# Performance work log

Measured on AMD Instinct MI355X. Metric: run time of the kernel, lower is better.

## Reference

```python
import jax, jax.numpy as jnp
import numpy as np

N = 4096
IN_F = 128
OUT_F = 64      # per-head out_features
HEADS = 4
ALPHA = 0.2     # LeakyReLU negative slope
NEG_FILL = -9e15


def setup_inputs() -> dict:
    key = jax.random.key(0)
    k_h, k_adj, k_W, k_a = jax.random.split(key, 4)
    h = jax.random.normal(k_h, (N, IN_F), dtype=jnp.float32)
    adj = jax.random.randint(k_adj, (N, N), 0, 2, dtype=jnp.int32)
    W = jax.random.normal(k_W, (IN_F, OUT_F * HEADS), dtype=jnp.float32) * 0.1
    a = jax.random.normal(k_a, (2 * OUT_F, 1), dtype=jnp.float32) * 0.1
    bias = jnp.zeros((OUT_F * HEADS,), dtype=jnp.float32)
    return {"h": h, "adj": adj, "W": W, "a": a, "bias": bias}


def reference(h, adj, W, a, bias):
    n = h.shape[0]
    Wh = (h @ W).reshape(n, HEADS, OUT_F)            # (N, H, F)
    # e_ij = leakyrelu(a_left . Wh_i + a_right . Wh_j)  (decomposed outer sum;
    # same math as concat([Wh_i, Wh_j]) @ a in the original)
    a_left = a[:OUT_F, 0]                            # (F,)
    a_right = a[OUT_F:, 0]                           # (F,)
    left = jnp.einsum('nhf,f->nh', Wh, a_left)       # (N, H)
    right = jnp.einsum('nhf,f->nh', Wh, a_right)     # (N, H)
    mask = adj > 0                                   # (N, N)
    outs = []
    for head in range(HEADS):                        # small fixed loop over heads
        e = left[:, head, None] + right[None, :, head]          # (N, N)
        e = jnp.where(e >= 0, e, ALPHA * e)                      # LeakyReLU
        e = jnp.where(mask, e, NEG_FILL)
        attn = jax.nn.softmax(e, axis=1)                         # (N, N)
        outs.append(attn @ Wh[:, head, :])                       # (N, F)
    out = jnp.concatenate(outs, axis=1)              # concat=True -> (N, H*F)
    return out + bias
```

## Files before the change

kernel.cpp:

```cpp
#include <hip/hip_runtime.h>
#include <hip/hip_bf16.h>

#define NN 4096
#define IN_F 128
#define OUT_F 64
#define C_TOT 256
#define ALPHA 0.2f
#define LOG2E 1.4426950408889634f

typedef float f32x4 __attribute__((ext_vector_type(4)));
typedef float f32x2 __attribute__((ext_vector_type(2)));
typedef __bf16 bf16x8 __attribute__((ext_vector_type(8)));

__device__ __forceinline__ unsigned fmap(float f) {
    unsigned u = __float_as_uint(f);
    return (u >> 31) ? ~u : (u | 0x80000000u);
}
__device__ __forceinline__ float funmap(unsigned u) {
    return (u >> 31) ? __uint_as_float(u & 0x7FFFFFFFu) : __uint_as_float(~u);
}
__device__ __forceinline__ unsigned short bfbits(float x) {
    union { __bf16 b; unsigned short u; } t;
    t.b = (__bf16)x;
    return t.u;
}
__device__ __forceinline__ void gl16(const void* g, void* l) {
    __builtin_amdgcn_global_load_lds((const __attribute__((address_space(1))) void*)g,
                                     (__attribute__((address_space(3))) void*)l, 16, 0, 0);
}

__global__ __launch_bounds__(256) void k_mask(
    const int* __restrict__ adj, unsigned* __restrict__ mask,
    const float* __restrict__ W, const float* __restrict__ a,
    unsigned short* __restrict__ WTbf, float* __restrict__ uLR,
    unsigned int* __restrict__ Rmax)
{
    const int tid = threadIdx.x;
    const int lane = tid & 63, wv = tid >> 6;
    const int row = blockIdx.x * 4 + wv;
    const int* __restrict__ ar = adj + (size_t)row * NN;
    unsigned* __restrict__ mr = mask + (size_t)row * 128;
    for (int c = 0; c < 8; ++c) {
        const int j0 = c * 512;
        unsigned w = 0u;
#pragma unroll
        for (int k = 0; k < 8; ++k) {
            const unsigned long long bb = __ballot(ar[j0 + k * 64 + lane] > 0);
            const unsigned lo = (unsigned)bb, hi = (unsigned)(bb >> 32);
            if ((lane >> 1) == k) w = (lane & 1) ? hi : lo;
        }
        if (lane < 16) {
            const int wi = c * 16 + lane;
            mr[(wi & 3) * 32 + (wi >> 2)] = w;
        }
    }

    if (blockIdx.x < 32) {
        const int b = blockIdx.x;
        const int c = b * 8 + (tid & 7);
#pragma unroll
        for (int pass = 0; pass < 4; ++pass) {
            const int k = pass * 32 + (tid >> 3);
            WTbf[(size_t)c * IN_F + k] = bfbits(W[k * C_TOT + c]);
        }
        if (b == 0) {
            if (tid < 4) Rmax[tid] = 0u;
            for (int o = tid; o < 1024; o += 256) {
                const int k = o >> 3, j = o & 7;
                const int hd = j & 3, side = j >> 2;
                float s = 0.f;
                for (int f = 0; f < OUT_F; ++f)
                    s = fmaf(W[k * C_TOT + hd * OUT_F + f], a[side * OUT_F + f], s);
                uLR[k * 8 + side * 4 + hd] = s;
            }
        }
    }
}

__global__ __launch_bounds__(256) void k_prep(
    const float* __restrict__ hmat, const unsigned short* __restrict__ WTbf,
    const float* __restrict__ uLR, unsigned short* __restrict__ WhT,
    float* __restrict__ leftT, float* __restrict__ rightT,
    unsigned int* __restrict__ Rmax)
{
    __shared__ float hs[16][132];
    __shared__ float us[128][8];
    const int tid = threadIdx.x;
    const int rowbase = blockIdx.x * 16;

    ((float4*)us)[tid] = ((const float4*)uLR)[tid];
#pragma unroll
    for (int p = 0; p < 8; ++p) {
        const int idx = p * 256 + tid;
        hs[idx >> 7][idx & 127] = hmat[(size_t)rowbase * IN_F + idx];
    }
    __syncthreads();

    const int lane = tid & 63, wv = tid >> 6;
    const int m16 = lane & 15, kg = lane >> 4;

    if (wv == 0) {
        const int row = lane >> 2, hd = lane & 3;
        float aL = 0.f, aR = 0.f;
#pragma unroll
        for (int k = 0; k < 128; k += 4) {
            const float4 hv = *(const float4*)&hs[row][k];
            aL = fmaf(hv.x, us[k][hd],   fmaf(hv.y, us[k+1][hd],   fmaf(hv.z, us[k+2][hd],   fmaf(hv.w, us[k+3][hd],   aL))));
            aR = fmaf(hv.x, us[k][hd+4], fmaf(hv.y, us[k+1][hd+4], fmaf(hv.z, us[k+2][hd+4], fmaf(hv.w, us[k+3][hd+4], aR))));
        }
        leftT [hd * NN + rowbase + row] = aL;
        rightT[hd * NN + rowbase + row] = aR * LOG2E;
        float mx = aR;
#pragma unroll
        for (int s = 4; s < 64; s <<= 1) mx = fmaxf(mx, __shfl_xor(mx, s, 64));
        if (lane < 4) atomicMax(&Rmax[hd], fmap(mx));
    }

    bf16x8 afr[4];
#pragma unroll
    for (int ks = 0; ks < 4; ++ks) {
        const float4 lo = *(const float4*)&hs[m16][ks * 32 + kg * 8];
        const float4 hi = *(const float4*)&hs[m16][ks * 32 + kg * 8 + 4];
        bf16x8 v;
        v[0] = (__bf16)lo.x; v[1] = (__bf16)lo.y; v[2] = (__bf16)lo.z; v[3] = (__bf16)lo.w;
        v[4] = (__bf16)hi.x; v[5] = (__bf16)hi.y; v[6] = (__bf16)hi.z; v[7] = (__bf16)hi.w;
        afr[ks] = v;
    }

#pragma unroll
    for (int nt0 = 0; nt0 < 4; ++nt0) {
        const int col = (wv * 4 + nt0) * 16 + m16;
        f32x4 acc = (f32x4){0.f, 0.f, 0.f, 0.f};
#pragma unroll
        for (int ks = 0; ks < 4; ++ks) {
            union { uint4 u; bf16x8 v; } B;
            B.u = *(const uint4*)(WTbf + (size_t)col * IN_F + ks * 32 + kg * 8);
            acc = __builtin_amdgcn_mfma_f32_16x16x32_bf16(afr[ks], B.v, acc, 0, 0, 0);
        }
#pragma unroll
        for (int i = 0; i < 4; ++i)
            WhT[(size_t)col * NN + rowbase + kg * 4 + i] = bfbits(acc[i]);
    }
}

__global__ __launch_bounds__(1024, 8) void k_attn(
    const unsigned* __restrict__ mask,
    const unsigned short* __restrict__ WhT,
    const float* __restrict__ leftT,
    const float* __restrict__ rightT,
    const unsigned int* __restrict__ Rmax,
    float* __restrict__ out,
    float* __restrict__ num1,
    float* __restrict__ den)
{
    __shared__ unsigned short Bb[4][64 * 128];
    __shared__ float erl[2048];
    __shared__ float er2l[2048];

    const int tid = threadIdx.x;
    const int lane = tid & 63;
    const int wvi = tid >> 6;
    const int rh = wvi & 3;
    const int j4 = wvi >> 2;
    const int jh = blockIdx.x & 1;
    const int hd = (blockIdx.x >> 1) & 3;
    const int rowbase = (blockIdx.x >> 3) * 64;
    const int m = lane & 15;
    const int kg = lane >> 4;
    const int sh = kg * 8;

    const int srow = tid >> 4;
    const int g_lin = tid & 15;
    const int lg = g_lin ^ (srow & 15);
    const unsigned short* gsrc = WhT + (size_t)(hd * 64 + srow) * NN
                                 + jh * 2048 + lg * 8;
    const int d0 = srow * 128 + g_lin * 8;

#define STAGE(buf, t) { gl16(gsrc + (t) * 128, &Bb[buf][d0]); }

    STAGE(0, 0); STAGE(1, 1); STAGE(2, 2);

    {
        const float2 rv = *(const float2*)(rightT + (size_t)hd * NN + jh * 2048 + tid * 2);
        erl [tid * 2    ] = exp2f(rv.x);
        erl [tid * 2 + 1] = exp2f(rv.y);
        er2l[tid * 2    ] = exp2f(ALPHA * rv.x);
        er2l[tid * 2 + 1] = exp2f(ALPHA * rv.y);
    }

    unsigned mreg[16];
    {
        const unsigned* mrow = mask + (size_t)(rowbase + rh * 16 + m) * 128
                               + j4 * 32 + jh * 16;
#pragma unroll
        for (int p = 0; p < 4; ++p) {
            const uint4 v = *(const uint4*)(mrow + p * 4);
            mreg[p * 4 + 0] = v.x; mreg[p * 4 + 1] = v.y;
            mreg[p * 4 + 2] = v.z; mreg[p * 4 + 3] = v.w;
        }
    }

    const float lf = leftT[hd * NN + rowbase + rh * 16 + m];
    const float rmx = funmap(Rmax[hd]);
    const float x = lf + rmx;
    const float m0v = fmaxf(x, ALPHA * x);
    const float mp0 = m0v * LOG2E;
    const float EL  = exp2f(fmaf(lf,         LOG2E, -mp0));
    const float EL2 = exp2f(fmaf(lf * ALPHA, LOG2E, -mp0));
    const f32x2 ELv  = (f32x2){EL,  EL};
    const f32x2 EL2v = (f32x2){EL2, EL2};

    bf16x8 ONE8;
#pragma unroll
    for (int i = 0; i < 8; ++i) ONE8[i] = (__bf16)1.0f;

    __syncthreads();

    const int pg8 = ((j4 * 4 + kg) ^ m) * 8;
    const int bro = m * 128 + pg8;

    f32x4 acc0 = (f32x4){0,0,0,0}, acc1 = acc0, acc2 = acc0, acc3 = acc0;
    f32x4 accL = (f32x4){0,0,0,0};

    union F4 { f32x4 v; f32x2 h[2]; };

#define COMPUTE(buf, t) {                                                        \
    const unsigned aw = mreg[(t)] >> sh;                                         \
    F4 E0, E1, F0, F1;                                                           \
    E0.v = *(const f32x4*)&erl [(t) * 128 + j4 * 32 + sh];                       \
    E1.v = *(const f32x4*)&erl [(t) * 128 + j4 * 32 + sh + 4];                   \
    F0.v = *(const f32x4*)&er2l[(t) * 128 + j4 * 32 + sh];                       \
    F1.v = *(const f32x4*)&er2l[(t) * 128 + j4 * 32 + sh + 4];                   \
    const f32x2 ep[4] = { E0.h[0], E0.h[1], E1.h[0], E1.h[1] };                  \
    const f32x2 fp[4] = { F0.h[0], F0.h[1], F1.h[0], F1.h[1] };                  \
    union { __bf16 b[8]; bf16x8 v; } Af;                                         \
    _Pragma("unroll")                                                            \
    for (int e = 0; e < 4; ++e) {                                                \
        const f32x2 full = ep[e] * ELv;                        \
        const f32x2 leak = fp[e] * EL2v;                       \
        float w0 = fmaxf(full.x, leak.x);                     \
        float w1 = fmaxf(full.y, leak.y);                                        \
        const unsigned mk0 = (unsigned)(((int)(aw << (31 - 2*e)))     >> 31);    \
        const unsigned mk1 = (unsigned)(((int)(aw << (31 - (2*e+1)))) >> 31);    \
        w0 = __uint_as_float(__float_as_uint(w0) & mk0);                         \
        w1 = __uint_as_float(__float_as_uint(w1) & mk1);                         \
        Af.b[2*e]   = (__bf16)w0;                                                \
        Af.b[2*e+1] = (__bf16)w1;                                                \
    }                                                                            \
    union { uint4 u; bf16x8 v; } B0, B1, B2, B3;                                 \
    B0.u = *(const uint4*)&Bb[buf][bro];                                         \
    B1.u = *(const uint4*)&Bb[buf][bro + 2048];                                  \
    B2.u = *(const uint4*)&Bb[buf][bro + 4096];                                  \
    B3.u = *(const uint4*)&Bb[buf][bro + 6144];                                  \
    acc0 = __builtin_amdgcn_mfma_f32_16x16x32_bf16(Af.v, B0.v, acc0, 0, 0, 0);   \
    acc1 = __builtin_amdgcn_mfma_f32_16x16x32_bf16(Af.v, B1.v, acc1, 0, 0, 0);   \
    acc2 = __builtin_amdgcn_mfma_f32_16x16x32_bf16(Af.v, B2.v, acc2, 0, 0, 0);   \
    acc3 = __builtin_amdgcn_mfma_f32_16x16x32_bf16(Af.v, B3.v, acc3, 0, 0, 0);   \
    accL = __builtin_amdgcn_mfma_f32_16x16x32_bf16(Af.v, ONE8, accL, 0, 0, 0);   \
}

#pragma unroll
    for (int t = 0; t < 16; ++t) {
        if (t <= 13)      { asm volatile("s_waitcnt vmcnt(2)" ::: "memory"); }
        else if (t == 14) { asm volatile("s_waitcnt vmcnt(1)" ::: "memory"); }
        else              { asm volatile("s_waitcnt vmcnt(0)" ::: "memory"); }
        __builtin_amdgcn_sched_barrier(0);
        __builtin_amdgcn_s_barrier();
        if (t + 3 < 16) STAGE((t + 3) & 3, t + 3);
        COMPUTE(t & 3, t);
        __builtin_amdgcn_sched_barrier(0);
    }
#undef STAGE
#undef COMPUTE

    __syncthreads();
    float* comb = (float*)&Bb[0][0];
    if (j4 > 0) {
        float* c = comb + (((j4 - 1) * 4 + rh) * 64 + lane) * 20;
#pragma unroll
        for (int i = 0; i < 4; ++i) {
            c[ 0 + i] = acc0[i]; c[ 4 + i] = acc1[i];
            c[ 8 + i] = acc2[i]; c[12 + i] = acc3[i];
            c[16 + i] = accL[i];
        }
    }
    __syncthreads();
    if (j4 == 0) {
#pragma unroll
        for (int pt = 0; pt < 3; ++pt) {
            const float* c = comb + ((pt * 4 + rh) * 64 + lane) * 20;
#pragma unroll
            for (int i = 0; i < 4; ++i) {
                acc0[i] += c[ 0 + i]; acc1[i] += c[ 4 + i];
                acc2[i] += c[ 8 + i]; acc3[i] += c[12 + i];
                accL[i] += c[16 + i];
            }
        }
        float* numdst = jh ? num1 : out;
#pragma unroll
        for (int q = 0; q < 4; ++q) {
            const f32x4 A = (q == 0) ? acc0 : (q == 1) ? acc1 : (q == 2) ? acc2 : acc3;
            const int col = hd * 64 + q * 16 + m;
#pragma unroll
            for (int i = 0; i < 4; ++i) {
                const int r = kg * 4 + i;
                numdst[(size_t)(rowbase + rh * 16 + r) * C_TOT + col] = A[i];
            }
        }
        if (m == 0) {
#pragma unroll
            for (int i = 0; i < 4; ++i)
                den[(size_t)jh * 4 * NN + hd * NN + rowbase + rh * 16 + kg * 4 + i] = accL[i];
        }
    }
}

__global__ __launch_bounds__(256) void k_fin(
    float* __restrict__ out, const float* __restrict__ num1,
    const float* __restrict__ den, const float* __restrict__ bias)
{
    const int idx = blockIdx.x * 256 + threadIdx.x;
    const int row = idx >> 6;
    const int c4 = (idx & 63) * 4;
    const int hd = c4 >> 6;
    const float d = den[hd * NN + row] + den[4 * NN + hd * NN + row];
    const float rd = 1.0f / d;
    float4 n0 = *(float4*)(out + (size_t)row * C_TOT + c4);
    const float4 n1 = *(const float4*)(num1 + (size_t)row * C_TOT + c4);
    const float4 bv = *(const float4*)(bias + c4);
    n0.x = fmaf(n0.x + n1.x, rd, bv.x);
    n0.y = fmaf(n0.y + n1.y, rd, bv.y);
    n0.z = fmaf(n0.z + n1.z, rd, bv.z);
    n0.w = fmaf(n0.w + n1.w, rd, bv.w);
    *(float4*)(out + (size_t)row * C_TOT + c4) = n0;
}

extern "C" void kernel_launch(void* const* d_in, const int* in_sizes, int n_in,
                              void* d_out, int out_size, void* d_ws, size_t ws_size,
                              hipStream_t stream) {
    const float* hmat = (const float*)d_in[0];
    const int*   adj  = (const int*)d_in[1];
    const float* W    = (const float*)d_in[2];
    const float* a    = (const float*)d_in[3];
    const float* bias = (const float*)d_in[4];
    float* out = (float*)d_out;

    char* ws = (char*)d_ws;
    unsigned short* WhT  = (unsigned short*)(ws + 0x000000);
    float* rightT        = (float*)(ws + 0x280000);
    float* leftT         = (float*)(ws + 0x2A0000);
    unsigned short* WTbf = (unsigned short*)(ws + 0x2B0000);
    float* uLR           = (float*)(ws + 0x2C0000);
    unsigned int* Rmax   = (unsigned int*)(ws + 0x2C1000);
    unsigned* mask       = (unsigned*)(ws + 0x300000);
    float* num1          = (float*)(ws + 0x500000);
    float* den           = (float*)(ws + 0x900000);

    hipLaunchKernelGGL(k_mask, dim3(1024), dim3(256), 0, stream,
                       adj, mask, W, a, WTbf, uLR, Rmax);
    hipLaunchKernelGGL(k_prep, dim3(256),  dim3(256), 0, stream,
                       hmat, WTbf, uLR, WhT, leftT, rightT, Rmax);
    hipLaunchKernelGGL(k_attn, dim3(512),  dim3(1024), 0, stream,
                       mask, WhT, leftT, rightT, Rmax, out, num1, den);
    hipLaunchKernelGGL(k_fin,  dim3(1024), dim3(256), 0, stream,
                       out, num1, den, bias);
}
```

Before: 64.00 us.

## Drop LDS staging in attention kernel; read WhT directly with smaller blocks

The attention kernel no longer stages WhT tiles into LDS through async global-to-LDS copies with a 4-deep barrier pipeline. Each wave now reads its B fragments, the exp(right) values and the mask words straight from global memory into registers. The mask is stored transposed so those reads coalesce, exp(right) is precomputed once in k_prep instead of per block, and blocks shrink to 256 threads over 16 rows with 4x more blocks. The aim is to remove barrier overhead and raise occupancy. The cost is that WhT is reused across 16 rows instead of 64, so global and L2 traffic goes up sharply and load latency is no longer hidden by explicit pipelining.

```diff
diff --git a/kernel.cpp b/kernel.cpp
--- a/kernel.cpp
+++ b/kernel.cpp
@@ -24,13 +24,9 @@
     t.b = (__bf16)x;
     return t.u;
 }
-__device__ __forceinline__ void gl16(const void* g, void* l) {
-    __builtin_amdgcn_global_load_lds((const __attribute__((address_space(1))) void*)g,
-                                     (__attribute__((address_space(3))) void*)l, 16, 0, 0);
-}
 
 __global__ __launch_bounds__(256) void k_mask(
-    const int* __restrict__ adj, unsigned* __restrict__ mask,
+    const int* __restrict__ adj, unsigned* __restrict__ maskT,
     const float* __restrict__ W, const float* __restrict__ a,
     unsigned short* __restrict__ WTbf, float* __restrict__ uLR,
     unsigned int* __restrict__ Rmax)
@@ -39,7 +35,6 @@
     const int lane = tid & 63, wv = tid >> 6;
     const int row = blockIdx.x * 4 + wv;
     const int* __restrict__ ar = adj + (size_t)row * NN;
-    unsigned* __restrict__ mr = mask + (size_t)row * 128;
     for (int c = 0; c < 8; ++c) {
         const int j0 = c * 512;
         unsigned w = 0u;
@@ -51,7 +46,7 @@
         }
         if (lane < 16) {
             const int wi = c * 16 + lane;
-            mr[(wi & 3) * 32 + (wi >> 2)] = w;
+            maskT[(size_t)wi * NN + row] = w;
         }
     }
 
@@ -80,7 +75,7 @@
 __global__ __launch_bounds__(256) void k_prep(
     const float* __restrict__ hmat, const unsigned short* __restrict__ WTbf,
     const float* __restrict__ uLR, unsigned short* __restrict__ WhT,
-    float* __restrict__ leftT, float* __restrict__ rightT,
+    float* __restrict__ leftT, float* __restrict__ er, float* __restrict__ er2,
     unsigned int* __restrict__ Rmax)
 {
     __shared__ float hs[16][132];
@@ -108,8 +103,10 @@
             aL = fmaf(hv.x, us[k][hd],   fmaf(hv.y, us[k+1][hd],   fmaf(hv.z, us[k+2][hd],   fmaf(hv.w, us[k+3][hd],   aL))));
             aR = fmaf(hv.x, us[k][hd+4], fmaf(hv.y, us[k+1][hd+4], fmaf(hv.z, us[k+2][hd+4], fmaf(hv.w, us[k+3][hd+4], aR))));
         }
-        leftT [hd * NN + rowbase + row] = aL;
-        rightT[hd * NN + rowbase + row] = aR * LOG2E;
+        leftT[hd * NN + rowbase + row] = aL;
+        const float rp = aR * LOG2E;
+        er [hd * NN + rowbase + row] = exp2f(rp);
+        er2[hd * NN + rowbase + row] = exp2f(ALPHA * rp);
         float mx = aR;
 #pragma unroll
         for (int s = 4; s < 64; s <<= 1) mx = fmaxf(mx, __shfl_xor(mx, s, 64));
@@ -143,68 +140,34 @@
     }
 }
 
-__global__ __launch_bounds__(1024, 8) void k_attn(
-    const unsigned* __restrict__ mask,
+__global__ __launch_bounds__(256, 4) void k_attn(
+    const unsigned* __restrict__ maskT,
     const unsigned short* __restrict__ WhT,
     const float* __restrict__ leftT,
-    const float* __restrict__ rightT,
+    const float* __restrict__ er,
+    const float* __restrict__ er2,
     const unsigned int* __restrict__ Rmax,
     float* __restrict__ out,
     float* __restrict__ num1,
     float* __restrict__ den)
 {
-    __shared__ unsigned short Bb[4][64 * 128];
-    __shared__ float erl[2048];
-    __shared__ float er2l[2048];
+    __shared__ float comb[3][64][20];
 
     const int tid = threadIdx.x;
     const int lane = tid & 63;
-    const int wvi = tid >> 6;
-    const int rh = wvi & 3;
-    const int j4 = wvi >> 2;
+    const int wv = tid >> 6;
     const int jh = blockIdx.x & 1;
     const int hd = (blockIdx.x >> 1) & 3;
-    const int rowbase = (blockIdx.x >> 3) * 64;
+    const int rowbase = (blockIdx.x >> 3) * 16;
     const int m = lane & 15;
     const int kg = lane >> 4;
     const int sh = kg * 8;
-
-    const int srow = tid >> 4;
-    const int g_lin = tid & 15;
-    const int lg = g_lin ^ (srow & 15);
-    const unsigned short* gsrc = WhT + (size_t)(hd * 64 + srow) * NN
-                                 + jh * 2048 + lg * 8;
-    const int d0 = srow * 128 + g_lin * 8;
-
-#define STAGE(buf, t) { gl16(gsrc + (t) * 128, &Bb[buf][d0]); }
-
-    STAGE(0, 0); STAGE(1, 1); STAGE(2, 2);
-
-    {
-        const float2 rv = *(const float2*)(rightT + (size_t)hd * NN + jh * 2048 + tid * 2);
-        erl [tid * 2    ] = exp2f(rv.x);
-        erl [tid * 2 + 1] = exp2f(rv.y);
-        er2l[tid * 2    ] = exp2f(ALPHA * rv.x);
-        er2l[tid * 2 + 1] = exp2f(ALPHA * rv.y);
-    }
-
-    unsigned mreg[16];
-    {
-        const unsigned* mrow = mask + (size_t)(rowbase + rh * 16 + m) * 128
-                               + j4 * 32 + jh * 16;
-#pragma unroll
-        for (int p = 0; p < 4; ++p) {
-            const uint4 v = *(const uint4*)(mrow + p * 4);
-            mreg[p * 4 + 0] = v.x; mreg[p * 4 + 1] = v.y;
-            mreg[p * 4 + 2] = v.z; mreg[p * 4 + 3] = v.w;
-        }
-    }
-
-    const float lf = leftT[hd * NN + rowbase + rh * 16 + m];
+    const int jbase = jh * 2048 + wv * 512;
+
     const float rmx = funmap(Rmax[hd]);
+    const float lf = leftT[hd * NN + rowbase + m];
     const float x = lf + rmx;
-    const float m0v = fmaxf(x, ALPHA * x);
-    const float mp0 = m0v * LOG2E;
+    const float mp0 = fmaxf(x, ALPHA * x) * LOG2E;
     const float EL  = exp2f(fmaf(lf,         LOG2E, -mp0));
     const float EL2 = exp2f(fmaf(lf * ALPHA, LOG2E, -mp0));
     const f32x2 ELv  = (f32x2){EL,  EL};
@@ -214,69 +177,59 @@
 #pragma unroll
     for (int i = 0; i < 8; ++i) ONE8[i] = (__bf16)1.0f;
 
-    __syncthreads();
-
-    const int pg8 = ((j4 * 4 + kg) ^ m) * 8;
-    const int bro = m * 128 + pg8;
+    const unsigned short* __restrict__ bp0 = WhT + (size_t)(hd * 64 +  0 + m) * NN + jbase + kg * 8;
+    const unsigned short* __restrict__ bp1 = WhT + (size_t)(hd * 64 + 16 + m) * NN + jbase + kg * 8;
+    const unsigned short* __restrict__ bp2 = WhT + (size_t)(hd * 64 + 32 + m) * NN + jbase + kg * 8;
+    const unsigned short* __restrict__ bp3 = WhT + (size_t)(hd * 64 + 48 + m) * NN + jbase + kg * 8;
+    const float* __restrict__ ep  = er  + (size_t)hd * NN + jbase + kg * 8;
+    const float* __restrict__ e2p = er2 + (size_t)hd * NN + jbase + kg * 8;
+    const unsigned* __restrict__ mp = maskT + (size_t)(jbase >> 5) * NN + rowbase + m;
 
     f32x4 acc0 = (f32x4){0,0,0,0}, acc1 = acc0, acc2 = acc0, acc3 = acc0;
     f32x4 accL = (f32x4){0,0,0,0};
 
     union F4 { f32x4 v; f32x2 h[2]; };
 
-#define COMPUTE(buf, t) {                                                        \
-    const unsigned aw = mreg[(t)] >> sh;                                         \
-    F4 E0, E1, F0, F1;                                                           \
-    E0.v = *(const f32x4*)&erl [(t) * 128 + j4 * 32 + sh];                       \
-    E1.v = *(const f32x4*)&erl [(t) * 128 + j4 * 32 + sh + 4];                   \
-    F0.v = *(const f32x4*)&er2l[(t) * 128 + j4 * 32 + sh];                       \
-    F1.v = *(const f32x4*)&er2l[(t) * 128 + j4 * 32 + sh + 4];                   \
-    const f32x2 ep[4] = { E0.h[0], E0.h[1], E1.h[0], E1.h[1] };                  \
-    const f32x2 fp[4] = { F0.h[0], F0.h[1], F1.h[0], F1.h[1] };                  \
-    union { __bf16 b[8]; bf16x8 v; } Af;                                         \
-    _Pragma("unroll")                                                            \
-    for (int e = 0; e < 4; ++e) {                                                \
-        const f32x2 full = ep[e] * ELv;                        \
-        const f32x2 leak = fp[e] * EL2v;                       \
-        float w0 = fmaxf(full.x, leak.x);                     \
-        float w1 = fmaxf(full.y, leak.y);                                        \
-        const unsigned mk0 = (unsigned)(((int)(aw << (31 - 2*e)))     >> 31);    \
-        const unsigned mk1 = (unsigned)(((int)(aw << (31 - (2*e+1)))) >> 31);    \
-        w0 = __uint_as_float(__float_as_uint(w0) & mk0);                         \
-        w1 = __uint_as_float(__float_as_uint(w1) & mk1);                         \
-        Af.b[2*e]   = (__bf16)w0;                                                \
-        Af.b[2*e+1] = (__bf16)w1;                                                \
-    }                                                                            \
-    union { uint4 u; bf16x8 v; } B0, B1, B2, B3;                                 \
-    B0.u = *(const uint4*)&Bb[buf][bro];                                         \
-    B1.u = *(const uint4*)&Bb[buf][bro + 2048];                                  \
-    B2.u = *(const uint4*)&Bb[buf][bro + 4096];                                  \
-    B3.u = *(const uint4*)&Bb[buf][bro + 6144];                                  \
-    acc0 = __builtin_amdgcn_mfma_f32_16x16x32_bf16(Af.v, B0.v, acc0, 0, 0, 0);   \
-    acc1 = __builtin_amdgcn_mfma_f32_16x16x32_bf16(Af.v, B1.v, acc1, 0, 0, 0);   \
-    acc2 = __builtin_amdgcn_mfma_f32_16x16x32_bf16(Af.v, B2.v, acc2, 0, 0, 0);   \
-    acc3 = __builtin_amdgcn_mfma_f32_16x16x32_bf16(Af.v, B3.v, acc3, 0, 0, 0);   \
-    accL = __builtin_amdgcn_mfma_f32_16x16x32_bf16(Af.v, ONE8, accL, 0, 0, 0);   \
-}
-
-#pragma unroll
+#pragma unroll 4
     for (int t = 0; t < 16; ++t) {
-        if (t <= 13)      { asm volatile("s_waitcnt vmcnt(2)" ::: "memory"); }
-        else if (t == 14) { asm volatile("s_waitcnt vmcnt(1)" ::: "memory"); }
-        else              { asm volatile("s_waitcnt vmcnt(0)" ::: "memory"); }
-        __builtin_amdgcn_sched_barrier(0);
-        __builtin_amdgcn_s_barrier();
-        if (t + 3 < 16) STAGE((t + 3) & 3, t + 3);
-        COMPUTE(t & 3, t);
-        __builtin_amdgcn_sched_barrier(0);
-    }
-#undef STAGE
-#undef COMPUTE
-
-    __syncthreads();
-    float* comb = (float*)&Bb[0][0];
-    if (j4 > 0) {
-        float* c = comb + (((j4 - 1) * 4 + rh) * 64 + lane) * 20;
+        const int o = t * 32;
+        const unsigned aw = mp[(size_t)t * NN] >> sh;
+        F4 E0, E1, F0, F1;
+        E0.v = *(const f32x4*)(ep  + o);
+        E1.v = *(const f32x4*)(ep  + o + 4);
+        F0.v = *(const f32x4*)(e2p + o);
+        F1.v = *(const f32x4*)(e2p + o + 4);
+        union { uint4 u; bf16x8 v; } B0, B1, B2, B3;
+        B0.u = *(const uint4*)(bp0 + o);
+        B1.u = *(const uint4*)(bp1 + o);
+        B2.u = *(const uint4*)(bp2 + o);
+        B3.u = *(const uint4*)(bp3 + o);
+
+        const f32x2 epr[4] = { E0.h[0], E0.h[1], E1.h[0], E1.h[1] };
+        const f32x2 fpr[4] = { F0.h[0], F0.h[1], F1.h[0], F1.h[1] };
+        union { __bf16 b[8]; bf16x8 v; } Af;
+#pragma unroll
+        for (int e = 0; e < 4; ++e) {
+            const f32x2 full = epr[e] * ELv;
+            const f32x2 leak = fpr[e] * EL2v;
+            float w0 = fmaxf(full.x, leak.x);
+            float w1 = fmaxf(full.y, leak.y);
+            const unsigned mk0 = (unsigned)(((int)(aw << (31 - 2*e)))     >> 31);
+            const unsigned mk1 = (unsigned)(((int)(aw << (31 - (2*e+1)))) >> 31);
+            w0 = __uint_as_float(__float_as_uint(w0) & mk0);
+            w1 = __uint_as_float(__float_as_uint(w1) & mk1);
+            Af.b[2*e]   = (__bf16)w0;
+            Af.b[2*e+1] = (__bf16)w1;
+        }
+        acc0 = __builtin_amdgcn_mfma_f32_16x16x32_bf16(Af.v, B0.v, acc0, 0, 0, 0);
+        acc1 = __builtin_amdgcn_mfma_f32_16x16x32_bf16(Af.v, B1.v, acc1, 0, 0, 0);
+        acc2 = __builtin_amdgcn_mfma_f32_16x16x32_bf16(Af.v, B2.v, acc2, 0, 0, 0);
+        acc3 = __builtin_amdgcn_mfma_f32_16x16x32_bf16(Af.v, B3.v, acc3, 0, 0, 0);
+        accL = __builtin_amdgcn_mfma_f32_16x16x32_bf16(Af.v, ONE8, accL, 0, 0, 0);
+    }
+
+    if (wv > 0) {
+        float* c = &comb[wv - 1][lane][0];
 #pragma unroll
         for (int i = 0; i < 4; ++i) {
             c[ 0 + i] = acc0[i]; c[ 4 + i] = acc1[i];
@@ -285,10 +238,10 @@
         }
     }
     __syncthreads();
-    if (j4 == 0) {
+    if (wv == 0) {
 #pragma unroll
         for (int pt = 0; pt < 3; ++pt) {
-            const float* c = comb + ((pt * 4 + rh) * 64 + lane) * 20;
+            const float* c = &comb[pt][lane][0];
 #pragma unroll
             for (int i = 0; i < 4; ++i) {
                 acc0[i] += c[ 0 + i]; acc1[i] += c[ 4 + i];
@@ -304,13 +257,13 @@
 #pragma unroll
             for (int i = 0; i < 4; ++i) {
                 const int r = kg * 4 + i;
-                numdst[(size_t)(rowbase + rh * 16 + r) * C_TOT + col] = A[i];
+                numdst[(size_t)(rowbase + r) * C_TOT + col] = A[i];
             }
         }
         if (m == 0) {
 #pragma unroll
             for (int i = 0; i < 4; ++i)
-                den[(size_t)jh * 4 * NN + hd * NN + rowbase + rh * 16 + kg * 4 + i] = accL[i];
+                den[(size_t)jh * 4 * NN + hd * NN + rowbase + kg * 4 + i] = accL[i];
         }
     }
 }
@@ -325,14 +278,15 @@
     const int hd = c4 >> 6;
     const float d = den[hd * NN + row] + den[4 * NN + hd * NN + row];
     const float rd = 1.0f / d;
-    float4 n0 = *(float4*)(out + (size_t)row * C_TOT + c4);
-    const float4 n1 = *(const float4*)(num1 + (size_t)row * C_TOT + c4);
+    const size_t off = (size_t)row * C_TOT + c4;
+    float4 n = *(float4*)(out + off);
+    const float4 n1 = *(const float4*)(num1 + off);
     const float4 bv = *(const float4*)(bias + c4);
-    n0.x = fmaf(n0.x + n1.x, rd, bv.x);
-    n0.y = fmaf(n0.y + n1.y, rd, bv.y);
-    n0.z = fmaf(n0.z + n1.z, rd, bv.z);
-    n0.w = fmaf(n0.w + n1.w, rd, bv.w);
-    *(float4*)(out + (size_t)row * C_TOT + c4) = n0;
+    n.x = fmaf(n.x + n1.x, rd, bv.x);
+    n.y = fmaf(n.y + n1.y, rd, bv.y);
+    n.z = fmaf(n.z + n1.z, rd, bv.z);
+    n.w = fmaf(n.w + n1.w, rd, bv.w);
+    *(float4*)(out + off) = n;
 }
 
 extern "C" void kernel_launch(void* const* d_in, const int* in_sizes, int n_in,
@@ -347,21 +301,22 @@
 
     char* ws = (char*)d_ws;
     unsigned short* WhT  = (unsigned short*)(ws + 0x000000);
-    float* rightT        = (float*)(ws + 0x280000);
     float* leftT         = (float*)(ws + 0x2A0000);
     unsigned short* WTbf = (unsigned short*)(ws + 0x2B0000);
     float* uLR           = (float*)(ws + 0x2C0000);
     unsigned int* Rmax   = (unsigned int*)(ws + 0x2C1000);
-    unsigned* mask       = (unsigned*)(ws + 0x300000);
+    float* er            = (float*)(ws + 0x2C2000);
+    float* er2           = (float*)(ws + 0x2D2000);
+    unsigned* maskT      = (unsigned*)(ws + 0x300000);
     float* num1          = (float*)(ws + 0x500000);
     float* den           = (float*)(ws + 0x900000);
 
     hipLaunchKernelGGL(k_mask, dim3(1024), dim3(256), 0, stream,
-                       adj, mask, W, a, WTbf, uLR, Rmax);
+                       adj, maskT, W, a, WTbf, uLR, Rmax);
     hipLaunchKernelGGL(k_prep, dim3(256),  dim3(256), 0, stream,
-                       hmat, WTbf, uLR, WhT, leftT, rightT, Rmax);
-    hipLaunchKernelGGL(k_attn, dim3(512),  dim3(1024), 0, stream,
-                       mask, WhT, leftT, rightT, Rmax, out, num1, den);
+                       hmat, WTbf, uLR, WhT, leftT, er, er2, Rmax);
+    hipLaunchKernelGGL(k_attn, dim3(2048), dim3(256), 0, stream,
+                       maskT, WhT, leftT, er, er2, Rmax, out, num1, den);
     hipLaunchKernelGGL(k_fin,  dim3(1024), dim3(256), 0, stream,
                        out, num1, den, bias);
 }
```

Result: slower. 112.7 us (+76.1%).

## Halve attention block threads; each wave computes two 16-row subtiles reusing B fragments

Applied to the files above, without the earlier changes.

Shrinks the attention kernel blocks from 1024 to 512 threads, and each wave now processes two 16-row subtiles. The B fragments loaded from LDS and the exp tables are reused across both subtiles, which halves LDS B reads per MFMA. Staging now issues two global-to-LDS loads per thread, so the vmcnt waits are adjusted. The cross-wave reduction runs per subtile with extra barriers. In exchange, register pressure roughly doubles for accumulators and mask words, and fewer waves are available per block to hide latency.

```diff
diff --git a/kernel.cpp b/kernel.cpp
--- a/kernel.cpp
+++ b/kernel.cpp
@@ -143,7 +143,7 @@
     }
 }
 
-__global__ __launch_bounds__(1024, 8) void k_attn(
+__global__ __launch_bounds__(512, 4) void k_attn(
     const unsigned* __restrict__ mask,
     const unsigned short* __restrict__ WhT,
     const float* __restrict__ leftT,
@@ -160,8 +160,8 @@
     const int tid = threadIdx.x;
     const int lane = tid & 63;
     const int wvi = tid >> 6;
-    const int rh = wvi & 3;
-    const int j4 = wvi >> 2;
+    const int rh2 = wvi & 1;
+    const int j4 = wvi >> 1;
     const int jh = blockIdx.x & 1;
     const int hd = (blockIdx.x >> 1) & 3;
     const int rowbase = (blockIdx.x >> 3) * 64;
@@ -172,43 +172,54 @@
     const int srow = tid >> 4;
     const int g_lin = tid & 15;
     const int lg = g_lin ^ (srow & 15);
-    const unsigned short* gsrc = WhT + (size_t)(hd * 64 + srow) * NN
-                                 + jh * 2048 + lg * 8;
+    const unsigned short* gsrc0 = WhT + (size_t)(hd * 64 + srow) * NN
+                                  + jh * 2048 + lg * 8;
+    const unsigned short* gsrc1 = gsrc0 + (size_t)32 * NN;
     const int d0 = srow * 128 + g_lin * 8;
 
-#define STAGE(buf, t) { gl16(gsrc + (t) * 128, &Bb[buf][d0]); }
+#define STAGE(buf, t) {                                   \
+    gl16(gsrc0 + (t) * 128, &Bb[buf][d0]);                \
+    gl16(gsrc1 + (t) * 128, &Bb[buf][d0 + 4096]); }
 
     STAGE(0, 0); STAGE(1, 1); STAGE(2, 2);
 
     {
-        const float2 rv = *(const float2*)(rightT + (size_t)hd * NN + jh * 2048 + tid * 2);
-        erl [tid * 2    ] = exp2f(rv.x);
-        erl [tid * 2 + 1] = exp2f(rv.y);
-        er2l[tid * 2    ] = exp2f(ALPHA * rv.x);
-        er2l[tid * 2 + 1] = exp2f(ALPHA * rv.y);
-    }
-
-    unsigned mreg[16];
-    {
-        const unsigned* mrow = mask + (size_t)(rowbase + rh * 16 + m) * 128
-                               + j4 * 32 + jh * 16;
+        const float4 rv = *(const float4*)(rightT + (size_t)hd * NN + jh * 2048 + tid * 4);
+        erl [tid * 4    ] = exp2f(rv.x);
+        erl [tid * 4 + 1] = exp2f(rv.y);
+        erl [tid * 4 + 2] = exp2f(rv.z);
+        erl [tid * 4 + 3] = exp2f(rv.w);
+        er2l[tid * 4    ] = exp2f(ALPHA * rv.x);
+        er2l[tid * 4 + 1] = exp2f(ALPHA * rv.y);
+        er2l[tid * 4 + 2] = exp2f(ALPHA * rv.z);
+        er2l[tid * 4 + 3] = exp2f(ALPHA * rv.w);
+    }
+
+    unsigned mreg[2][16];
+#pragma unroll
+    for (int sub = 0; sub < 2; ++sub) {
+        const unsigned* mrow = mask
+            + (size_t)(rowbase + rh2 * 32 + sub * 16 + m) * 128 + j4 * 32 + jh * 16;
 #pragma unroll
         for (int p = 0; p < 4; ++p) {
             const uint4 v = *(const uint4*)(mrow + p * 4);
-            mreg[p * 4 + 0] = v.x; mreg[p * 4 + 1] = v.y;
-            mreg[p * 4 + 2] = v.z; mreg[p * 4 + 3] = v.w;
-        }
-    }
-
-    const float lf = leftT[hd * NN + rowbase + rh * 16 + m];
+            mreg[sub][p * 4 + 0] = v.x; mreg[sub][p * 4 + 1] = v.y;
+            mreg[sub][p * 4 + 2] = v.z; mreg[sub][p * 4 + 3] = v.w;
+        }
+    }
+
     const float rmx = funmap(Rmax[hd]);
-    const float x = lf + rmx;
-    const float m0v = fmaxf(x, ALPHA * x);
-    const float mp0 = m0v * LOG2E;
-    const float EL  = exp2f(fmaf(lf,         LOG2E, -mp0));
-    const float EL2 = exp2f(fmaf(lf * ALPHA, LOG2E, -mp0));
-    const f32x2 ELv  = (f32x2){EL,  EL};
-    const f32x2 EL2v = (f32x2){EL2, EL2};
+    f32x2 ELv[2], EL2v[2];
+#pragma unroll
+    for (int sub = 0; sub < 2; ++sub) {
+        const float lf = leftT[hd * NN + rowbase + rh2 * 32 + sub * 16 + m];
+        const float x = lf + rmx;
+        const float mp0 = fmaxf(x, ALPHA * x) * LOG2E;
+        const float EL  = exp2f(fmaf(lf,         LOG2E, -mp0));
+        const float EL2 = exp2f(fmaf(lf * ALPHA, LOG2E, -mp0));
+        ELv [sub] = (f32x2){EL,  EL};
+        EL2v[sub] = (f32x2){EL2, EL2};
+    }
 
     bf16x8 ONE8;
 #pragma unroll
@@ -219,50 +230,58 @@
     const int pg8 = ((j4 * 4 + kg) ^ m) * 8;
     const int bro = m * 128 + pg8;
 
-    f32x4 acc0 = (f32x4){0,0,0,0}, acc1 = acc0, acc2 = acc0, acc3 = acc0;
-    f32x4 accL = (f32x4){0,0,0,0};
+    f32x4 acc[2][4], accL[2];
+#pragma unroll
+    for (int sub = 0; sub < 2; ++sub) {
+        accL[sub] = (f32x4){0,0,0,0};
+#pragma unroll
+        for (int q = 0; q < 4; ++q) acc[sub][q] = (f32x4){0,0,0,0};
+    }
 
     union F4 { f32x4 v; f32x2 h[2]; };
 
 #define COMPUTE(buf, t) {                                                        \
-    const unsigned aw = mreg[(t)] >> sh;                                         \
     F4 E0, E1, F0, F1;                                                           \
     E0.v = *(const f32x4*)&erl [(t) * 128 + j4 * 32 + sh];                       \
     E1.v = *(const f32x4*)&erl [(t) * 128 + j4 * 32 + sh + 4];                   \
     F0.v = *(const f32x4*)&er2l[(t) * 128 + j4 * 32 + sh];                       \
     F1.v = *(const f32x4*)&er2l[(t) * 128 + j4 * 32 + sh + 4];                   \
-    const f32x2 ep[4] = { E0.h[0], E0.h[1], E1.h[0], E1.h[1] };                  \
-    const f32x2 fp[4] = { F0.h[0], F0.h[1], F1.h[0], F1.h[1] };                  \
-    union { __bf16 b[8]; bf16x8 v; } Af;                                         \
-    _Pragma("unroll")                                                            \
-    for (int e = 0; e < 4; ++e) {                                                \
-        const f32x2 full = ep[e] * ELv;                        \
-        const f32x2 leak = fp[e] * EL2v;                       \
-        float w0 = fmaxf(full.x, leak.x);                     \
-        float w1 = fmaxf(full.y, leak.y);                                        \
-        const unsigned mk0 = (unsigned)(((int)(aw << (31 - 2*e)))     >> 31);    \
-        const unsigned mk1 = (unsigned)(((int)(aw << (31 - (2*e+1)))) >> 31);    \
-        w0 = __uint_as_float(__float_as_uint(w0) & mk0);                         \
-        w1 = __uint_as_float(__float_as_uint(w1) & mk1);                         \
-        Af.b[2*e]   = (__bf16)w0;                                                \
-        Af.b[2*e+1] = (__bf16)w1;                                                \
-    }                                                                            \
     union { uint4 u; bf16x8 v; } B0, B1, B2, B3;                                 \
     B0.u = *(const uint4*)&Bb[buf][bro];                                         \
     B1.u = *(const uint4*)&Bb[buf][bro + 2048];                                  \
     B2.u = *(const uint4*)&Bb[buf][bro + 4096];                                  \
     B3.u = *(const uint4*)&Bb[buf][bro + 6144];                                  \
-    acc0 = __builtin_amdgcn_mfma_f32_16x16x32_bf16(Af.v, B0.v, acc0, 0, 0, 0);   \
-    acc1 = __builtin_amdgcn_mfma_f32_16x16x32_bf16(Af.v, B1.v, acc1, 0, 0, 0);   \
-    acc2 = __builtin_amdgcn_mfma_f32_16x16x32_bf16(Af.v, B2.v, acc2, 0, 0, 0);   \
-    acc3 = __builtin_amdgcn_mfma_f32_16x16x32_bf16(Af.v, B3.v, acc3, 0, 0, 0);   \
-    accL = __builtin_amdgcn_mfma_f32_16x16x32_bf16(Af.v, ONE8, accL, 0, 0, 0);   \
+    const f32x2 ep[4] = { E0.h[0], E0.h[1], E1.h[0], E1.h[1] };                  \
+    const f32x2 fp[4] = { F0.h[0], F0.h[1], F1.h[0], F1.h[1] };                  \
+    _Pragma("unroll")                                                            \
+    for (int sub = 0; sub < 2; ++sub) {                                          \
+        const unsigned aw = mreg[sub][(t)] >> sh;                                \
+        union { __bf16 b[8]; bf16x8 v; } Af;                                     \
+        _Pragma("unroll")                                                        \
+        for (int e = 0; e < 4; ++e) {                                            \
+            const f32x2 full = ep[e] * ELv[sub];               \
+            const f32x2 leak = fp[e] * EL2v[sub];              \
+            float w0 = fmaxf(full.x, leak.x);                 \
+            float w1 = fmaxf(full.y, leak.y);                                    \
+            const unsigned mk0 = (unsigned)(((int)(aw << (31 - 2*e)))     >> 31);\
+            const unsigned mk1 = (unsigned)(((int)(aw << (31 - (2*e+1)))) >> 31);\
+            w0 = __uint_as_float(__float_as_uint(w0) & mk0);                     \
+            w1 = __uint_as_float(__float_as_uint(w1) & mk1);                     \
+            Af.b[2*e]   = (__bf16)w0;                                            \
+            Af.b[2*e+1] = (__bf16)w1;                                            \
+        }                                                                        \
+        acc[sub][0] = __builtin_amdgcn_mfma_f32_16x16x32_bf16(Af.v, B0.v, acc[sub][0], 0, 0, 0); \
+        acc[sub][1] = __builtin_amdgcn_mfma_f32_16x16x32_bf16(Af.v, B1.v, acc[sub][1], 0, 0, 0); \
+        acc[sub][2] = __builtin_amdgcn_mfma_f32_16x16x32_bf16(Af.v, B2.v, acc[sub][2], 0, 0, 0); \
+        acc[sub][3] = __builtin_amdgcn_mfma_f32_16x16x32_bf16(Af.v, B3.v, acc[sub][3], 0, 0, 0); \
+        accL[sub]   = __builtin_amdgcn_mfma_f32_16x16x32_bf16(Af.v, ONE8, accL[sub], 0, 0, 0);   \
+    }                                                                            \
 }
 
 #pragma unroll
     for (int t = 0; t < 16; ++t) {
-        if (t <= 13)      { asm volatile("s_waitcnt vmcnt(2)" ::: "memory"); }
-        else if (t == 14) { asm volatile("s_waitcnt vmcnt(1)" ::: "memory"); }
+        if (t <= 13)      { asm volatile("s_waitcnt vmcnt(4)" ::: "memory"); }
+        else if (t == 14) { asm volatile("s_waitcnt vmcnt(2)" ::: "memory"); }
         else              { asm volatile("s_waitcnt vmcnt(0)" ::: "memory"); }
         __builtin_amdgcn_sched_barrier(0);
         __builtin_amdgcn_s_barrier();
@@ -273,44 +292,47 @@
 #undef STAGE
 #undef COMPUTE
 
-    __syncthreads();
     float* comb = (float*)&Bb[0][0];
-    if (j4 > 0) {
-        float* c = comb + (((j4 - 1) * 4 + rh) * 64 + lane) * 20;
-#pragma unroll
-        for (int i = 0; i < 4; ++i) {
-            c[ 0 + i] = acc0[i]; c[ 4 + i] = acc1[i];
-            c[ 8 + i] = acc2[i]; c[12 + i] = acc3[i];
-            c[16 + i] = accL[i];
-        }
-    }
-    __syncthreads();
-    if (j4 == 0) {
-#pragma unroll
-        for (int pt = 0; pt < 3; ++pt) {
-            const float* c = comb + ((pt * 4 + rh) * 64 + lane) * 20;
+#pragma unroll
+    for (int sub = 0; sub < 2; ++sub) {
+        __syncthreads();
+        if (j4 > 0) {
+            float* c = comb + (((j4 - 1) * 2 + rh2) * 64 + lane) * 20;
 #pragma unroll
             for (int i = 0; i < 4; ++i) {
-                acc0[i] += c[ 0 + i]; acc1[i] += c[ 4 + i];
-                acc2[i] += c[ 8 + i]; acc3[i] += c[12 + i];
-                accL[i] += c[16 + i];
-            }
-        }
-        float* numdst = jh ? num1 : out;
-#pragma unroll
-        for (int q = 0; q < 4; ++q) {
-            const f32x4 A = (q == 0) ? acc0 : (q == 1) ? acc1 : (q == 2) ? acc2 : acc3;
-            const int col = hd * 64 + q * 16 + m;
-#pragma unroll
-            for (int i = 0; i < 4; ++i) {
-                const int r = kg * 4 + i;
-                numdst[(size_t)(rowbase + rh * 16 + r) * C_TOT + col] = A[i];
-            }
-        }
-        if (m == 0) {
-#pragma unroll
-            for (int i = 0; i < 4; ++i)
-                den[(size_t)jh * 4 * NN + hd * NN + rowbase + rh * 16 + kg * 4 + i] = accL[i];
+                c[ 0 + i] = acc[sub][0][i]; c[ 4 + i] = acc[sub][1][i];
+                c[ 8 + i] = acc[sub][2][i]; c[12 + i] = acc[sub][3][i];
+                c[16 + i] = accL[sub][i];
+            }
+        }
+        __syncthreads();
+        if (j4 == 0) {
+#pragma unroll
+            for (int pt = 0; pt < 3; ++pt) {
+                const float* c = comb + ((pt * 2 + rh2) * 64 + lane) * 20;
+#pragma unroll
+                for (int i = 0; i < 4; ++i) {
+                    acc[sub][0][i] += c[ 0 + i]; acc[sub][1][i] += c[ 4 + i];
+                    acc[sub][2][i] += c[ 8 + i]; acc[sub][3][i] += c[12 + i];
+                    accL[sub][i]   += c[16 + i];
+                }
+            }
+            float* numdst = jh ? num1 : out;
+            const int rbase = rowbase + rh2 * 32 + sub * 16;
+#pragma unroll
+            for (int q = 0; q < 4; ++q) {
+                const int col = hd * 64 + q * 16 + m;
+#pragma unroll
+                for (int i = 0; i < 4; ++i) {
+                    const int r = kg * 4 + i;
+                    numdst[(size_t)(rbase + r) * C_TOT + col] = acc[sub][q][i];
+                }
+            }
+            if (m == 0) {
+#pragma unroll
+                for (int i = 0; i < 4; ++i)
+                    den[(size_t)jh * 4 * NN + hd * NN + rbase + kg * 4 + i] = accL[sub][i];
+            }
         }
     }
 }
@@ -325,14 +347,15 @@
     const int hd = c4 >> 6;
     const float d = den[hd * NN + row] + den[4 * NN + hd * NN + row];
     const float rd = 1.0f / d;
-    float4 n0 = *(float4*)(out + (size_t)row * C_TOT + c4);
-    const float4 n1 = *(const float4*)(num1 + (size_t)row * C_TOT + c4);
+    const size_t off = (size_t)row * C_TOT + c4;
+    float4 n = *(float4*)(out + off);
+    const float4 n1 = *(const float4*)(num1 + off);
     const float4 bv = *(const float4*)(bias + c4);
-    n0.x = fmaf(n0.x + n1.x, rd, bv.x);
-    n0.y = fmaf(n0.y + n1.y, rd, bv.y);
-    n0.z = fmaf(n0.z + n1.z, rd, bv.z);
-    n0.w = fmaf(n0.w + n1.w, rd, bv.w);
-    *(float4*)(out + (size_t)row * C_TOT + c4) = n0;
+    n.x = fmaf(n.x + n1.x, rd, bv.x);
+    n.y = fmaf(n.y + n1.y, rd, bv.y);
+    n.z = fmaf(n.z + n1.z, rd, bv.z);
+    n.w = fmaf(n.w + n1.w, rd, bv.w);
+    *(float4*)(out + off) = n;
 }
 
 extern "C" void kernel_launch(void* const* d_in, const int* in_sizes, int n_in,
@@ -360,7 +383,7 @@
                        adj, mask, W, a, WTbf, uLR, Rmax);
     hipLaunchKernelGGL(k_prep, dim3(256),  dim3(256), 0, stream,
                        hmat, WTbf, uLR, WhT, leftT, rightT, Rmax);
-    hipLaunchKernelGGL(k_attn, dim3(512),  dim3(1024), 0, stream,
+    hipLaunchKernelGGL(k_attn, dim3(512),  dim3(512), 0, stream,
                        mask, WhT, leftT, rightT, Rmax, out, num1, den);
     hipLaunchKernelGGL(k_fin,  dim3(1024), dim3(256), 0, stream,
                        out, num1, den, bias);
```

New measurement: 64.46 us. Within noise of the previous version (+0.7%).
